# Kernel optimization log

Measured on AMD Instinct MI355X. Metric: run time of the kernel, lower is better.

The kernel has to match this reference:

```python
import jax, jax.numpy as jnp
import numpy as np

B, Z, H, T = 4096, 512, 384, 32


def setup_inputs() -> dict:
    key = jax.random.key(0)
    ks = jax.random.split(key, 8)
    z = jax.random.normal(ks[0], (B, Z), dtype=jnp.float32)
    h_init = jax.random.normal(ks[1], (B, H), dtype=jnp.float32) * 0.01
    s1 = 1.0 / np.sqrt(Z)
    s23 = 1.0 / np.sqrt(2 * H)
    W1 = jax.random.uniform(ks[2], (H, Z), jnp.float32, -s1, s1)
    b1 = jax.random.uniform(ks[3], (H,), jnp.float32, -s1, s1)
    W2 = jax.random.uniform(ks[4], (Z, 2 * H), jnp.float32, -s23, s23)
    b2 = jax.random.uniform(ks[5], (Z,), jnp.float32, -s23, s23)
    W3 = jax.random.uniform(ks[6], (H, 2 * H), jnp.float32, -s23, s23)
    b3 = jax.random.uniform(ks[7], (H,), jnp.float32, -s23, s23)
    return {"z": z, "h_init": h_init, "W1": W1, "b1": b1, "W2": W2,
            "b2": b2, "W3": W3, "b3": b3, "n_frames": T}


def reference(z, h_init, W1, b1, W2, b2, W3, b3, n_frames):
    # training path: r = w_residual*4 / n_frames (const decay)
    r = jnp.asarray(0.2 * 4.0 / n_frames, dtype=z.dtype)
    lrelu = lambda x: jax.nn.leaky_relu(x, 0.01)

    def step(carry, _):
        zp, hp = carry
        temp = jnp.concatenate([lrelu(zp @ W1.T + b1), hp], axis=-1)  # [B, 2H]
        zn = lrelu(temp @ W2.T + b2) * r + zp
        hn = lrelu(temp @ W3.T + b3) * r + hp
        return (zn, hn), zn

    _, outs = jax.lax.scan(step, (z, h_init), None, length=n_frames - 1)
    all_out = jnp.concatenate([z[None], outs], axis=0)        # [T, B, Z]
    out = (all_out - z[None]).transpose(1, 0, 2)               # [B, T, Z]
    return out.reshape(-1, z.shape[-1])                        # [B*T, Z]
```

## Files before the change

### kernel.cpp

```cpp
#include <hip/hip_runtime.h>
#include <type_traits>


typedef _Float16 f16;
typedef f16 f16x8 __attribute__((ext_vector_type(8)));
typedef float f32x4 __attribute__((ext_vector_type(4)));
typedef float f32x16 __attribute__((ext_vector_type(16)));

#define ZD 512
#define HD 384
#define TT 32
#define BM 32
#define LZ 516
#define LT 392

__device__ __forceinline__ float lrelu(float x) { return x >= 0.f ? x : 0.01f * x; }

__global__ void cvt_f32_f16(const float* __restrict__ s, f16* __restrict__ d, int n) {
    for (int i = blockIdx.x * blockDim.x + threadIdx.x; i < n; i += gridDim.x * blockDim.x)
        d[i] = (f16)s[i];
}

__global__ __launch_bounds__(512) void latrec(
    const float* __restrict__ z0g, const float* __restrict__ h0g,
    const f16* __restrict__ W1h, const f16* __restrict__ W2h, const f16* __restrict__ W3h,
    const float* __restrict__ b1g, const float* __restrict__ b2g, const float* __restrict__ b3g,
    float* __restrict__ out)
{
    __shared__ float zf[BM * LZ];
    __shared__ f16 tz[BM * LT];
    __shared__ f16 hb[2][BM * LT];
    __shared__ float bias[1280];

    const int tid = threadIdx.x;
    const int w = tid >> 6, l = tid & 63;
    const int lm = l & 31;
    const int lk = (l >> 5) * 8;
    const int m0 = blockIdx.x * BM;

    for (int i = tid; i < HD; i += 512) bias[i] = b1g[i];
    for (int i = tid; i < ZD; i += 512) bias[384 + i] = b2g[i];
    for (int i = tid; i < HD; i += 512) bias[896 + i] = b3g[i];
    for (int i = tid; i < BM * 128; i += 512) {
        int r = i >> 7, c = (i & 127) << 2;
        f32x4 v = *(const f32x4*)(z0g + (size_t)(m0 + r) * ZD + c);
        *(f32x4*)(zf + r * LZ + c) = v;
        f32x4 zr = {0.f, 0.f, 0.f, 0.f};
        __builtin_nontemporal_store(zr.x, out + ((size_t)(m0 + r) * TT) * ZD + c);
        __builtin_nontemporal_store(zr.y, out + ((size_t)(m0 + r) * TT) * ZD + c + 1);
        __builtin_nontemporal_store(zr.z, out + ((size_t)(m0 + r) * TT) * ZD + c + 2);
        __builtin_nontemporal_store(zr.w, out + ((size_t)(m0 + r) * TT) * ZD + c + 3);
    }
    for (int i = tid; i < BM * HD; i += 512) {
        int r = i / HD, c = i - r * HD;
        hb[0][r * LT + c] = (f16)h0g[(size_t)(m0 + r) * HD + c];
    }
    __syncthreads();

    for (int t = 1; t < TT; ++t) {
        const f16* hcur = hb[(t - 1) & 1];
        f16* hnxt = hb[t & 1];

        {
            const int nt0 = (w < 4) ? 2 * w : (w + 4);
            const int nt1 = (w < 4) ? 2 * w + 1 : nt0;
            const float* ap = zf + lm * LZ + lk;
            const f16* wp0 = W1h + (size_t)(nt0 * 32 + lm) * ZD + lk;
            const f16* wp1 = W1h + (size_t)(nt1 * 32 + lm) * ZD + lk;
            auto run1 = [&](auto NTC) {
                constexpr int NT = decltype(NTC)::value;
                f32x16 a0 = {}, a1 = {};
                #pragma unroll 4
                for (int ks = 0; ks < ZD; ks += 16) {
                    f32x4 x0 = *(const f32x4*)(ap + ks);
                    f32x4 x1 = *(const f32x4*)(ap + ks + 4);
                    f16x8 af;
                    #pragma unroll
                    for (int e = 0; e < 4; ++e) { af[e] = (f16)x0[e]; af[4 + e] = (f16)x1[e]; }
                    f16x8 bf0 = *(const f16x8*)(wp0 + ks);
                    a0 = __builtin_amdgcn_mfma_f32_32x32x16_f16(af, bf0, a0, 0, 0, 0);
                    if constexpr (NT == 2) {
                        f16x8 bf1 = *(const f16x8*)(wp1 + ks);
                        a1 = __builtin_amdgcn_mfma_f32_32x32x16_f16(af, bf1, a1, 0, 0, 0);
                    }
                }
                {
                    int c = nt0 * 32 + lm; float bv = bias[c];
                    #pragma unroll
                    for (int rg = 0; rg < 16; ++rg) {
                        int row = (rg & 3) + 8 * (rg >> 2) + 4 * (l >> 5);
                        tz[row * LT + c] = (f16)lrelu(a0[rg] + bv);
                    }
                }
                if constexpr (NT == 2) {
                    int c = nt1 * 32 + lm; float bv = bias[c];
                    #pragma unroll
                    for (int rg = 0; rg < 16; ++rg) {
                        int row = (rg & 3) + 8 * (rg >> 2) + 4 * (l >> 5);
                        tz[row * LT + c] = (f16)lrelu(a1[rg] + bv);
                    }
                }
            };
            if (w < 4) run1(std::integral_constant<int, 2>{});
            else       run1(std::integral_constant<int, 1>{});
        }
        __syncthreads();

        {
            const int t0 = w, t1 = w + 8;
            const int t2 = (w < 4) ? 16 + 2 * w : 20 + w;
            const int t3 = (w < 4) ? 17 + 2 * w : t2;
            auto wptr = [&](int nt) {
                return (nt < 16) ? W2h + (size_t)(nt * 32 + lm) * 768 + lk
                                 : W3h + (size_t)((nt - 16) * 32 + lm) * 768 + lk;
            };
            const f16* wp0 = wptr(t0); const f16* wp1 = wptr(t1);
            const f16* wp2 = wptr(t2); const f16* wp3 = wptr(t3);
            const f16* ap1 = tz + lm * LT + lk;
            const f16* ap2 = hcur + lm * LT + lk;

            auto epi2 = [&](const f32x16& ac, int nt) {
                if (nt < 16) {
                    int c = nt * 32 + lm;
                    float bv = bias[384 + c];
                    #pragma unroll
                    for (int rg = 0; rg < 16; ++rg) {
                        int row = (rg & 3) + 8 * (rg >> 2) + 4 * (l >> 5);
                        float v = lrelu(ac[rg] + bv) * 0.025f;
                        float zn = zf[row * LZ + c] + v;
                        zf[row * LZ + c] = zn;
                        size_t gr = (size_t)(m0 + row);
                        float o = zn - z0g[gr * ZD + c];
                        __builtin_nontemporal_store(o, out + (gr * TT + t) * ZD + c);
                    }
                } else {
                    int c = (nt - 16) * 32 + lm;
                    float bv = bias[896 + c];
                    #pragma unroll
                    for (int rg = 0; rg < 16; ++rg) {
                        int row = (rg & 3) + 8 * (rg >> 2) + 4 * (l >> 5);
                        float v = lrelu(ac[rg] + bv) * 0.025f;
                        float hn = (float)hcur[row * LT + c] + v;
                        hnxt[row * LT + c] = (f16)hn;
                    }
                }
            };

            auto run2 = [&](auto NTC) {
                constexpr int NT = decltype(NTC)::value;
                f32x16 a0 = {}, a1 = {}, a2 = {}, a3 = {};
                auto khalf = [&](const f16* ab, int kw) {
                    #pragma unroll 4
                    for (int ks = 0; ks < HD; ks += 16) {
                        f16x8 af = *(const f16x8*)(ab + ks);
                        f16x8 b0 = *(const f16x8*)(wp0 + kw + ks);
                        a0 = __builtin_amdgcn_mfma_f32_32x32x16_f16(af, b0, a0, 0, 0, 0);
                        f16x8 b1 = *(const f16x8*)(wp1 + kw + ks);
                        a1 = __builtin_amdgcn_mfma_f32_32x32x16_f16(af, b1, a1, 0, 0, 0);
                        f16x8 b2 = *(const f16x8*)(wp2 + kw + ks);
                        a2 = __builtin_amdgcn_mfma_f32_32x32x16_f16(af, b2, a2, 0, 0, 0);
                        if constexpr (NT == 4) {
                            f16x8 b3 = *(const f16x8*)(wp3 + kw + ks);
                            a3 = __builtin_amdgcn_mfma_f32_32x32x16_f16(af, b3, a3, 0, 0, 0);
                        }
                    }
                };
                khalf(ap1, 0);
                khalf(ap2, HD);
                epi2(a0, t0); epi2(a1, t1); epi2(a2, t2);
                if constexpr (NT == 4) epi2(a3, t3);
            };
            if (w < 4) run2(std::integral_constant<int, 4>{});
            else       run2(std::integral_constant<int, 3>{});
        }
        __syncthreads();
    }
}

extern "C" void kernel_launch(void* const* d_in, const int* in_sizes, int n_in,
                              void* d_out, int out_size, void* d_ws, size_t ws_size,
                              hipStream_t stream) {
    const float* z  = (const float*)d_in[0];
    const float* h0 = (const float*)d_in[1];
    const float* W1 = (const float*)d_in[2];
    const float* b1 = (const float*)d_in[3];
    const float* W2 = (const float*)d_in[4];
    const float* b2 = (const float*)d_in[5];
    const float* W3 = (const float*)d_in[6];
    const float* b3 = (const float*)d_in[7];
    float* out = (float*)d_out;

    char* p = (char*)d_ws;
    f16* W1h = (f16*)p; p += (size_t)HD * ZD * 2;
    f16* W2h = (f16*)p; p += (size_t)ZD * 768 * 2;
    f16* W3h = (f16*)p; p += (size_t)HD * 768 * 2;

    cvt_f32_f16<<<96, 256, 0, stream>>>(W1, W1h, HD * ZD);
    cvt_f32_f16<<<192, 256, 0, stream>>>(W2, W2h, ZD * 768);
    cvt_f32_f16<<<144, 256, 0, stream>>>(W3, W3h, HD * 768);

    latrec<<<4096 / BM, 512, 0, stream>>>(z, h0, W1h, W2h, W3h, b1, b2, b3, out);
}
```

Before: 1.835 ms.

## Halve batch tile, switch to 16x16x32 MFMA with register-resident state and prefetch

```diff
diff --git a/kernel.cpp b/kernel.cpp
--- a/kernel.cpp
+++ b/kernel.cpp
@@ -5,12 +5,12 @@
 typedef _Float16 f16;
 typedef f16 f16x8 __attribute__((ext_vector_type(8)));
 typedef float f32x4 __attribute__((ext_vector_type(4)));
-typedef float f32x16 __attribute__((ext_vector_type(16)));
 
 #define ZD 512
 #define HD 384
+#define K2 768
 #define TT 32
-#define BM 32
+#define BM 16
 #define LZ 516
 #define LT 392
 
@@ -30,30 +30,56 @@
     __shared__ float zf[BM * LZ];
     __shared__ f16 tz[BM * LT];
     __shared__ f16 hb[2][BM * LT];
-    __shared__ float bias[1280];
 
     const int tid = threadIdx.x;
     const int w = tid >> 6, l = tid & 63;
-    const int lm = l & 31;
-    const int lk = (l >> 5) * 8;
+    const int lm = l & 15;
+    const int k0 = (l >> 4) * 8;
+    const int rg0 = (l >> 4) * 4;
     const int m0 = blockIdx.x * BM;
 
-    for (int i = tid; i < HD; i += 512) bias[i] = b1g[i];
-    for (int i = tid; i < ZD; i += 512) bias[384 + i] = b2g[i];
-    for (int i = tid; i < HD; i += 512) bias[896 + i] = b3g[i];
     for (int i = tid; i < BM * 128; i += 512) {
         int r = i >> 7, c = (i & 127) << 2;
         f32x4 v = *(const f32x4*)(z0g + (size_t)(m0 + r) * ZD + c);
         *(f32x4*)(zf + r * LZ + c) = v;
-        f32x4 zr = {0.f, 0.f, 0.f, 0.f};
-        __builtin_nontemporal_store(zr.x, out + ((size_t)(m0 + r) * TT) * ZD + c);
-        __builtin_nontemporal_store(zr.y, out + ((size_t)(m0 + r) * TT) * ZD + c + 1);
-        __builtin_nontemporal_store(zr.z, out + ((size_t)(m0 + r) * TT) * ZD + c + 2);
-        __builtin_nontemporal_store(zr.w, out + ((size_t)(m0 + r) * TT) * ZD + c + 3);
-    }
-    for (int i = tid; i < BM * HD; i += 512) {
-        int r = i / HD, c = i - r * HD;
-        hb[0][r * LT + c] = (f16)h0g[(size_t)(m0 + r) * HD + c];
+        float* op = out + (size_t)(m0 + r) * TT * ZD + c;
+        __builtin_nontemporal_store(0.f, op + 0);
+        __builtin_nontemporal_store(0.f, op + 1);
+        __builtin_nontemporal_store(0.f, op + 2);
+        __builtin_nontemporal_store(0.f, op + 3);
+    }
+
+    int c1[3], cz[4], ch[3];
+    float bv1[3], bvz[4], bvh[3];
+    float hreg[3][4], rfz[4][4];
+    const f16* w1p[3];
+    const f16* wp[7];
+    #pragma unroll
+    for (int j = 0; j < 3; ++j) {
+        c1[j] = (w + 8 * j) * 16 + lm;
+        bv1[j] = b1g[c1[j]];
+        w1p[j] = W1h + (size_t)c1[j] * ZD + k0;
+    }
+    #pragma unroll
+    for (int i = 0; i < 4; ++i) {
+        cz[i] = (w + 8 * i) * 16 + lm;
+        bvz[i] = b2g[cz[i]];
+        wp[i] = W2h + (size_t)cz[i] * K2 + k0;
+        #pragma unroll
+        for (int r = 0; r < 4; ++r) rfz[i][r] = 0.f;
+    }
+    #pragma unroll
+    for (int i = 0; i < 3; ++i) {
+        ch[i] = (w + 8 * i) * 16 + lm;
+        bvh[i] = b3g[ch[i]];
+        wp[4 + i] = W3h + (size_t)ch[i] * K2 + k0;
+        #pragma unroll
+        for (int r = 0; r < 4; ++r) {
+            int row = rg0 + r;
+            float hv = h0g[(size_t)(m0 + row) * HD + ch[i]];
+            hreg[i][r] = hv;
+            hb[0][row * LT + ch[i]] = (f16)hv;
+        }
     }
     __syncthreads();
 
@@ -62,116 +88,101 @@
         f16* hnxt = hb[t & 1];
 
         {
-            const int nt0 = (w < 4) ? 2 * w : (w + 4);
-            const int nt1 = (w < 4) ? 2 * w + 1 : nt0;
-            const float* ap = zf + lm * LZ + lk;
-            const f16* wp0 = W1h + (size_t)(nt0 * 32 + lm) * ZD + lk;
-            const f16* wp1 = W1h + (size_t)(nt1 * 32 + lm) * ZD + lk;
-            auto run1 = [&](auto NTC) {
-                constexpr int NT = decltype(NTC)::value;
-                f32x16 a0 = {}, a1 = {};
-                #pragma unroll 4
-                for (int ks = 0; ks < ZD; ks += 16) {
-                    f32x4 x0 = *(const f32x4*)(ap + ks);
-                    f32x4 x1 = *(const f32x4*)(ap + ks + 4);
-                    f16x8 af;
-                    #pragma unroll
-                    for (int e = 0; e < 4; ++e) { af[e] = (f16)x0[e]; af[4 + e] = (f16)x1[e]; }
-                    f16x8 bf0 = *(const f16x8*)(wp0 + ks);
-                    a0 = __builtin_amdgcn_mfma_f32_32x32x16_f16(af, bf0, a0, 0, 0, 0);
-                    if constexpr (NT == 2) {
-                        f16x8 bf1 = *(const f16x8*)(wp1 + ks);
-                        a1 = __builtin_amdgcn_mfma_f32_32x32x16_f16(af, bf1, a1, 0, 0, 0);
-                    }
-                }
-                {
-                    int c = nt0 * 32 + lm; float bv = bias[c];
-                    #pragma unroll
-                    for (int rg = 0; rg < 16; ++rg) {
-                        int row = (rg & 3) + 8 * (rg >> 2) + 4 * (l >> 5);
-                        tz[row * LT + c] = (f16)lrelu(a0[rg] + bv);
-                    }
-                }
-                if constexpr (NT == 2) {
-                    int c = nt1 * 32 + lm; float bv = bias[c];
-                    #pragma unroll
-                    for (int rg = 0; rg < 16; ++rg) {
-                        int row = (rg & 3) + 8 * (rg >> 2) + 4 * (l >> 5);
-                        tz[row * LT + c] = (f16)lrelu(a1[rg] + bv);
-                    }
-                }
-            };
-            if (w < 4) run1(std::integral_constant<int, 2>{});
-            else       run1(std::integral_constant<int, 1>{});
+            f32x4 ac[3] = {};
+            const float* ap = zf + lm * LZ + k0;
+            f16x8 cb[3];
+            #pragma unroll
+            for (int j = 0; j < 3; ++j) cb[j] = *(const f16x8*)(w1p[j]);
+            #pragma unroll 4
+            for (int ks = 0; ks < 15; ++ks) {
+                f32x4 x0 = *(const f32x4*)(ap + ks * 32);
+                f32x4 x1 = *(const f32x4*)(ap + ks * 32 + 4);
+                f16x8 af;
+                #pragma unroll
+                for (int e = 0; e < 4; ++e) { af[e] = (f16)x0[e]; af[4 + e] = (f16)x1[e]; }
+                f16x8 nb[3];
+                #pragma unroll
+                for (int j = 0; j < 3; ++j) nb[j] = *(const f16x8*)(w1p[j] + (ks + 1) * 32);
+                #pragma unroll
+                for (int j = 0; j < 3; ++j)
+                    ac[j] = __builtin_amdgcn_mfma_f32_16x16x32_f16(af, cb[j], ac[j], 0, 0, 0);
+                #pragma unroll
+                for (int j = 0; j < 3; ++j) cb[j] = nb[j];
+            }
+            {
+                f32x4 x0 = *(const f32x4*)(ap + 15 * 32);
+                f32x4 x1 = *(const f32x4*)(ap + 15 * 32 + 4);
+                f16x8 af;
+                #pragma unroll
+                for (int e = 0; e < 4; ++e) { af[e] = (f16)x0[e]; af[4 + e] = (f16)x1[e]; }
+                #pragma unroll
+                for (int j = 0; j < 3; ++j)
+                    ac[j] = __builtin_amdgcn_mfma_f32_16x16x32_f16(af, cb[j], ac[j], 0, 0, 0);
+            }
+            #pragma unroll
+            for (int j = 0; j < 3; ++j) {
+                #pragma unroll
+                for (int r = 0; r < 4; ++r)
+                    tz[(rg0 + r) * LT + c1[j]] = (f16)lrelu(ac[j][r] + bv1[j]);
+            }
         }
         __syncthreads();
 
         {
-            const int t0 = w, t1 = w + 8;
-            const int t2 = (w < 4) ? 16 + 2 * w : 20 + w;
-            const int t3 = (w < 4) ? 17 + 2 * w : t2;
-            auto wptr = [&](int nt) {
-                return (nt < 16) ? W2h + (size_t)(nt * 32 + lm) * 768 + lk
-                                 : W3h + (size_t)((nt - 16) * 32 + lm) * 768 + lk;
+            f32x4 ac[7] = {};
+            f16x8 cb[7];
+            #pragma unroll
+            for (int j = 0; j < 7; ++j) cb[j] = *(const f16x8*)(wp[j]);
+            const f16* apz = tz + lm * LT + k0;
+            const f16* aph = hcur + lm * LT + k0;
+
+            auto khalf = [&](const f16* ap, int kw, auto TAILC) {
+                constexpr bool TAIL = decltype(TAILC)::value;
+                constexpr int NS = TAIL ? 11 : 12;
+                #pragma unroll 4
+                for (int ks = 0; ks < NS; ++ks) {
+                    f16x8 af = *(const f16x8*)(ap + ks * 32);
+                    f16x8 nb[7];
+                    #pragma unroll
+                    for (int j = 0; j < 7; ++j) nb[j] = *(const f16x8*)(wp[j] + kw + (ks + 1) * 32);
+                    #pragma unroll
+                    for (int j = 0; j < 7; ++j)
+                        ac[j] = __builtin_amdgcn_mfma_f32_16x16x32_f16(af, cb[j], ac[j], 0, 0, 0);
+                    #pragma unroll
+                    for (int j = 0; j < 7; ++j) cb[j] = nb[j];
+                }
+                if constexpr (TAIL) {
+                    f16x8 af = *(const f16x8*)(ap + 11 * 32);
+                    #pragma unroll
+                    for (int j = 0; j < 7; ++j)
+                        ac[j] = __builtin_amdgcn_mfma_f32_16x16x32_f16(af, cb[j], ac[j], 0, 0, 0);
+                }
             };
-            const f16* wp0 = wptr(t0); const f16* wp1 = wptr(t1);
-            const f16* wp2 = wptr(t2); const f16* wp3 = wptr(t3);
-            const f16* ap1 = tz + lm * LT + lk;
-            const f16* ap2 = hcur + lm * LT + lk;
-
-            auto epi2 = [&](const f32x16& ac, int nt) {
-                if (nt < 16) {
-                    int c = nt * 32 + lm;
-                    float bv = bias[384 + c];
-                    #pragma unroll
-                    for (int rg = 0; rg < 16; ++rg) {
-                        int row = (rg & 3) + 8 * (rg >> 2) + 4 * (l >> 5);
-                        float v = lrelu(ac[rg] + bv) * 0.025f;
-                        float zn = zf[row * LZ + c] + v;
-                        zf[row * LZ + c] = zn;
-                        size_t gr = (size_t)(m0 + row);
-                        float o = zn - z0g[gr * ZD + c];
-                        __builtin_nontemporal_store(o, out + (gr * TT + t) * ZD + c);
-                    }
-                } else {
-                    int c = (nt - 16) * 32 + lm;
-                    float bv = bias[896 + c];
-                    #pragma unroll
-                    for (int rg = 0; rg < 16; ++rg) {
-                        int row = (rg & 3) + 8 * (rg >> 2) + 4 * (l >> 5);
-                        float v = lrelu(ac[rg] + bv) * 0.025f;
-                        float hn = (float)hcur[row * LT + c] + v;
-                        hnxt[row * LT + c] = (f16)hn;
-                    }
-                }
-            };
-
-            auto run2 = [&](auto NTC) {
-                constexpr int NT = decltype(NTC)::value;
-                f32x16 a0 = {}, a1 = {}, a2 = {}, a3 = {};
-                auto khalf = [&](const f16* ab, int kw) {
-                    #pragma unroll 4
-                    for (int ks = 0; ks < HD; ks += 16) {
-                        f16x8 af = *(const f16x8*)(ab + ks);
-                        f16x8 b0 = *(const f16x8*)(wp0 + kw + ks);
-                        a0 = __builtin_amdgcn_mfma_f32_32x32x16_f16(af, b0, a0, 0, 0, 0);
-                        f16x8 b1 = *(const f16x8*)(wp1 + kw + ks);
-                        a1 = __builtin_amdgcn_mfma_f32_32x32x16_f16(af, b1, a1, 0, 0, 0);
-                        f16x8 b2 = *(const f16x8*)(wp2 + kw + ks);
-                        a2 = __builtin_amdgcn_mfma_f32_32x32x16_f16(af, b2, a2, 0, 0, 0);
-                        if constexpr (NT == 4) {
-                            f16x8 b3 = *(const f16x8*)(wp3 + kw + ks);
-                            a3 = __builtin_amdgcn_mfma_f32_32x32x16_f16(af, b3, a3, 0, 0, 0);
-                        }
-                    }
-                };
-                khalf(ap1, 0);
-                khalf(ap2, HD);
-                epi2(a0, t0); epi2(a1, t1); epi2(a2, t2);
-                if constexpr (NT == 4) epi2(a3, t3);
-            };
-            if (w < 4) run2(std::integral_constant<int, 4>{});
-            else       run2(std::integral_constant<int, 3>{});
+            khalf(apz, 0, std::integral_constant<bool, false>{});
+            khalf(aph, 384, std::integral_constant<bool, true>{});
+
+            #pragma unroll
+            for (int i = 0; i < 4; ++i) {
+                #pragma unroll
+                for (int r = 0; r < 4; ++r) {
+                    int row = rg0 + r;
+                    float v = lrelu(ac[i][r] + bvz[i]) * 0.025f;
+                    rfz[i][r] += v;
+                    zf[row * LZ + cz[i]] += v;
+                    __builtin_nontemporal_store(rfz[i][r],
+                        out + ((size_t)(m0 + row) * TT + t) * ZD + cz[i]);
+                }
+            }
+            #pragma unroll
+            for (int i = 0; i < 3; ++i) {
+                #pragma unroll
+                for (int r = 0; r < 4; ++r) {
+                    int row = rg0 + r;
+                    float v = lrelu(ac[4 + i][r] + bvh[i]) * 0.025f;
+                    hreg[i][r] += v;
+                    hnxt[row * LT + ch[i]] = (f16)hreg[i][r];
+                }
+            }
         }
         __syncthreads();
     }
@@ -192,12 +203,12 @@
 
     char* p = (char*)d_ws;
     f16* W1h = (f16*)p; p += (size_t)HD * ZD * 2;
-    f16* W2h = (f16*)p; p += (size_t)ZD * 768 * 2;
-    f16* W3h = (f16*)p; p += (size_t)HD * 768 * 2;
+    f16* W2h = (f16*)p; p += (size_t)ZD * K2 * 2;
+    f16* W3h = (f16*)p; p += (size_t)HD * K2 * 2;
 
     cvt_f32_f16<<<96, 256, 0, stream>>>(W1, W1h, HD * ZD);
-    cvt_f32_f16<<<192, 256, 0, stream>>>(W2, W2h, ZD * 768);
-    cvt_f32_f16<<<144, 256, 0, stream>>>(W3, W3h, HD * 768);
+    cvt_f32_f16<<<192, 256, 0, stream>>>(W2, W2h, ZD * K2);
+    cvt_f32_f16<<<144, 256, 0, stream>>>(W3, W3h, HD * K2);
 
     latrec<<<4096 / BM, 512, 0, stream>>>(z, h0, W1h, W2h, W3h, b1, b2, b3, out);
 }
```

After: 2.578 ms. +40.4%, slower.
